# Optimization experiments

Hardware: AMD Instinct MI355X
Metric: run time of the kernel (lower is better)

Reference implementation:

```python
import jax, jax.numpy as jnp
import numpy as np

DIM, E, K, H = 512, 8, 2, 16  # hidden_dim is hardcoded to 16 in the torch module
B, N = 8, 4096
BN_EPS = 1e-5


def setup_inputs() -> dict:
    key = jax.random.key(0)
    ks = jax.random.split(key, 12)
    s = 0.02
    return {
        "x": jax.random.normal(ks[0], (B, N, DIM), jnp.float32),
        # gate: Conv1d(dim, dim, 1) -> weight [dim, dim]; BatchNorm1d(dim); Conv1d(dim, E, 1)
        "wg1": jax.random.normal(ks[1], (DIM, DIM), jnp.float32) * s,
        "bg1": jnp.zeros((DIM,), jnp.float32),
        "gamma": jnp.ones((DIM,), jnp.float32),
        "beta": jnp.zeros((DIM,), jnp.float32),
        "wg2": jax.random.normal(ks[2], (E, DIM), jnp.float32) * s,
        "bg2": jnp.zeros((E,), jnp.float32),
        # experts stacked: Linear(dim,16) -> w1 [E, dim, 16]; Linear(16,dim) -> w2 [E, 16, dim]
        "w1": jax.random.normal(ks[3], (E, DIM, H), jnp.float32) * s,
        "b1": jnp.zeros((E, H), jnp.float32),
        "w2": jax.random.normal(ks[4], (E, H, DIM), jnp.float32) * s,
        "b2": jnp.zeros((E, DIM), jnp.float32),
    }


def reference(x, wg1, bg1, gamma, beta, wg2, bg2, w1, b1, w2, b2):
    b, n, c = x.shape
    t = b * n
    flat = x.reshape(t, c)                                 # [T, C]

    # gate: 1x1 conv == per-token linear; BN over all tokens per channel (train-mode batch stats)
    h = flat @ wg1.T + bg1                                  # [T, C]
    mu = h.mean(axis=0)
    var = h.var(axis=0)                                     # biased, matches torch BN normalization
    h = gamma * (h - mu) * jax.lax.rsqrt(var + BN_EPS) + beta
    h = jax.nn.relu(h)
    logits = h @ wg2.T + bg2                                # [T, E]

    vals, idx = jax.lax.top_k(logits, K)                    # [T, K]
    topk_w = jax.nn.softmax(vals, axis=-1)
    weight = jnp.zeros((t, logits.shape[-1]), logits.dtype)
    weight = weight.at[jnp.arange(t)[:, None], idx].set(topk_w)  # scatter, [T, E]

    # dense expert compute for every token (faithful to original)
    h1 = jax.nn.relu(jnp.einsum('tc,ech->teh', flat, w1) + b1)   # [T, E, H]
    all_out = jnp.einsum('teh,ehc->tec', h1, w2) + b2            # [T, E, C]
    out_flat = jnp.einsum('tec,te->tc', all_out, weight)         # masked combine

    out = out_flat.reshape(b, n, c).transpose(0, 2, 1)           # [B, C, N]
    usage = weight.sum(axis=0) / t
    lb_loss = (usage ** 2).sum() * logits.shape[-1]
    return out, lb_loss
```

## Files before the change

### kernel.cpp

```cpp
#include <hip/hip_runtime.h>

#define T_TOK 32768
#define C_DIM 512
#define N_SEQ 4096

typedef unsigned short ushort_t;
typedef unsigned int uint_t;
typedef __attribute__((ext_vector_type(8))) _Float16 half8;
typedef __attribute__((ext_vector_type(4))) float f32x4;

static __device__ __forceinline__ ushort_t f2h_bits(float f) {
  _Float16 h = (_Float16)f;
  return __builtin_bit_cast(ushort_t, h);
}
static __device__ __forceinline__ float h_bits2f(ushort_t u) {
  return (float)__builtin_bit_cast(_Float16, u);
}

static __device__ __forceinline__ half8 frag_ld(const ushort_t* base, int r, int q) {
  const int off = r * 32 + ((q ^ ((r >> 1) & 3)) * 8);
  return *(const half8*)(base + off);
}

#define GLOAD_LDS(gptr, lptr)                                                  \
  __builtin_amdgcn_global_load_lds(                                            \
      (const __attribute__((address_space(1))) uint_t*)(gptr),                 \
      (__attribute__((address_space(3))) uint_t*)(lptr), 16, 0, 0)

__global__ __launch_bounds__(256) void prep(
    const float* __restrict__ wg1, const float* __restrict__ w1,
    const float* __restrict__ w2, const float* __restrict__ b2,
    ushort_t* __restrict__ Whi, ushort_t* __restrict__ Wlo,
    ushort_t* __restrict__ W1t, ushort_t* __restrict__ W2t,
    float* __restrict__ stats, float* __restrict__ usage,
    uint_t* __restrict__ done) {
  const int idx = blockIdx.x * 256 + threadIdx.x;
  {
    const float v = wg1[idx];
    const ushort_t h = f2h_bits(v);
    Whi[idx] = h;
    Wlo[idx] = f2h_bits(v - h_bits2f(h));
  }
  if (idx < 65536) {
    const int eh = idx >> 9, c = idx & 511;
    const int e = eh >> 4, hh = eh & 15;
    W1t[idx] = f2h_bits(w1[((size_t)e * 512 + c) * 16 + hh]);
  }
  if (idx < 81920) {
    const int c = idx / 160, k = idx - c * 160;
    float v = 0.f;
    if (k < 128) {
      const int e = k >> 4, hh = k & 15;
      v = w2[((size_t)e * 16 + hh) * 512 + c];
    } else if (k < 136) {
      v = b2[(size_t)(k - 128) * 512 + c];
    }
    W2t[c * 160 + k] = f2h_bits(v);
  }
  if (blockIdx.x == 1023) {
    float4 z = {0.f, 0.f, 0.f, 0.f};
    *(float4*)&stats[threadIdx.x * 4] = z;
    if (threadIdx.x < 8) usage[threadIdx.x] = 0.f;
    if (threadIdx.x == 8) *done = 0u;
  }
}

__global__ __launch_bounds__(256) void k1_mfma(
    const float* __restrict__ X, const ushort_t* __restrict__ Whi,
    const ushort_t* __restrict__ Wlo, const float* __restrict__ bg1,
    float* __restrict__ H, float* __restrict__ stats) {
  __shared__ ushort_t sAh[4096], sAl[4096], sBh[4096], sBl[4096];
  const int tid = threadIdx.x, lane = tid & 63, w = tid >> 6;
  const int wm = w >> 1, wn = w & 1;
  const int b = blockIdx.x;
  const int m0 = ((b & 7) | ((b >> 5) << 3)) * 128;
  const int n0 = ((b >> 3) & 3) * 128;
  const int cl = lane & 15, qf = lane >> 4;

  const int p1 = tid, p2 = tid + 256;
  const int r1 = p1 >> 2, q1 = (p1 & 3) ^ ((r1 >> 1) & 3);
  const int r2 = p2 >> 2, q2 = (p2 & 3) ^ ((r2 >> 1) & 3);
  const float* xb1 = X + (size_t)(m0 + r1) * 512 + q1 * 8;
  const float* xb2 = X + (size_t)(m0 + r2) * 512 + q2 * 8;

  float4 xr[4];
#define K1_LOADX(kc)                                                           \
  {                                                                            \
    const int kk = (kc) * 32;                                                  \
    xr[0] = *(const float4*)(xb1 + kk);                                        \
    xr[1] = *(const float4*)(xb1 + kk + 4);                                    \
    xr[2] = *(const float4*)(xb2 + kk);                                        \
    xr[3] = *(const float4*)(xb2 + kk + 4);                                    \
  }

  K1_LOADX(0);
  f32x4 acc[4][4] = {};

  for (int kc = 0; kc < 16; ++kc) {
    const int k0 = kc * 32;
    __syncthreads();
#pragma unroll
    for (int j = 0; j < 2; ++j) {
      const int pb = (w * 2 + j) * 64 + lane;
      const int rb = pb >> 2, qb = (pb & 3) ^ ((rb >> 1) & 3);
      GLOAD_LDS(Whi + (size_t)(n0 + rb) * 512 + k0 + qb * 8, sBh + pb * 8);
      GLOAD_LDS(Wlo + (size_t)(n0 + rb) * 512 + k0 + qb * 8, sBl + pb * 8);
    }
    {
      ushort_t hi[16], lo[16];
      const float* v = (const float*)xr;
#pragma unroll
      for (int j = 0; j < 16; ++j) {
        hi[j] = f2h_bits(v[j]);
        lo[j] = f2h_bits(v[j] - h_bits2f(hi[j]));
      }
      *(uint4*)(sAh + p1 * 8) = *(uint4*)(hi);
      *(uint4*)(sAl + p1 * 8) = *(uint4*)(lo);
      *(uint4*)(sAh + p2 * 8) = *(uint4*)(hi + 8);
      *(uint4*)(sAl + p2 * 8) = *(uint4*)(lo + 8);
    }
    __syncthreads();
    if (kc < 15) K1_LOADX(kc + 1);

    half8 ah[4], al[4], bh[4], bl[4];
#pragma unroll
    for (int f = 0; f < 4; ++f) {
      ah[f] = frag_ld(sAh, wm * 64 + f * 16 + cl, qf);
      al[f] = frag_ld(sAl, wm * 64 + f * 16 + cl, qf);
      bh[f] = frag_ld(sBh, wn * 64 + f * 16 + cl, qf);
      bl[f] = frag_ld(sBl, wn * 64 + f * 16 + cl, qf);
    }
#pragma unroll
    for (int i = 0; i < 4; ++i)
#pragma unroll
      for (int j = 0; j < 4; ++j) {
        acc[i][j] = __builtin_amdgcn_mfma_f32_16x16x32_f16(ah[i], bh[j], acc[i][j], 0, 0, 0);
        acc[i][j] = __builtin_amdgcn_mfma_f32_16x16x32_f16(ah[i], bl[j], acc[i][j], 0, 0, 0);
        acc[i][j] = __builtin_amdgcn_mfma_f32_16x16x32_f16(al[i], bh[j], acc[i][j], 0, 0, 0);
      }
  }
#undef K1_LOADX

  float s[4] = {0, 0, 0, 0}, qs[4] = {0, 0, 0, 0};
  const int rq = lane >> 4;
#pragma unroll
  for (int nf = 0; nf < 4; ++nf) {
    const int col = n0 + wn * 64 + nf * 16 + cl;
    const float bv = bg1[col];
#pragma unroll
    for (int mf = 0; mf < 4; ++mf) {
      const int row = m0 + wm * 64 + mf * 16 + rq * 4;
#pragma unroll
      for (int i = 0; i < 4; ++i) {
        const float v = acc[mf][nf][i] + bv;
        H[(size_t)(row + i) * 512 + col] = v;
        s[nf] += v;
        qs[nf] += v * v;
      }
    }
  }
#pragma unroll
  for (int nf = 0; nf < 4; ++nf) {
    s[nf] += __shfl_xor(s[nf], 16, 64);
    qs[nf] += __shfl_xor(qs[nf], 16, 64);
    s[nf] += __shfl_xor(s[nf], 32, 64);
    qs[nf] += __shfl_xor(qs[nf], 32, 64);
  }
  if (lane < 16) {
#pragma unroll
    for (int nf = 0; nf < 4; ++nf) {
      const int col = n0 + wn * 64 + nf * 16 + cl;
      atomicAdd(&stats[col], s[nf]);
      atomicAdd(&stats[512 + col], qs[nf]);
    }
  }
}

__global__ __launch_bounds__(256) void k5_fused(
    const float* __restrict__ X, const ushort_t* __restrict__ W1t,
    const ushort_t* __restrict__ W2t, const float* __restrict__ b1,
    const float* __restrict__ H, const float* __restrict__ stats,
    const float* __restrict__ gamma, const float* __restrict__ beta,
    const float* __restrict__ wg2, const float* __restrict__ bg2,
    float* __restrict__ usage, uint_t* __restrict__ done,
    float* __restrict__ Out) {
  __shared__ ushort_t sA[2][2048];
  __shared__ ushort_t Pl[64 * 168];
  __shared__ float wtab[64 * 8];
  __shared__ float ys[128 * 68];
  __shared__ float scsh_l[1024];
  __shared__ float lus[8];

  const int tid = threadIdx.x, lane = tid & 63, w = tid >> 6;
  const int wm = w >> 1, wn = w & 1;
  const int t0 = blockIdx.x * 64;
  const int bi = t0 >> 12, n0 = t0 & 4095;
  const int cl = lane & 15, qf = lane >> 4, rq = lane >> 4;

  const int pA = tid, rA = pA >> 2, qA = (pA & 3) ^ ((rA >> 1) & 3);
  const float* xbase = X + (size_t)(t0 + rA) * 512 + qA * 8;
  float4 xq0 = *(const float4*)(xbase);
  float4 xq1 = *(const float4*)(xbase + 4);

  if (tid < 8) lus[tid] = 0.f;
  wtab[tid] = 0.f;
  wtab[tid + 256] = 0.f;
  {
    uint4 z = {0, 0, 0, 0};
    const int row = tid >> 2, hf = tid & 3;
    *(uint4*)&Pl[row * 168 + 128 + hf * 8] = z;
  }
#pragma unroll
  for (int rep = 0; rep < 2; ++rep) {
    const int c = tid + rep * 256;
    const double mu = (double)stats[c] * (1.0 / (double)T_TOK);
    const double var = (double)stats[512 + c] * (1.0 / (double)T_TOK) - mu * mu;
    const double rstd = 1.0 / sqrt(var + 1e-5);
    const float scv = (float)((double)gamma[c] * rstd);
    scsh_l[c] = scv;
    scsh_l[512 + c] = beta[c] - (float)mu * scv;
  }
  __syncthreads();

  {
    const int cb = lane * 8;
    float sc[8], sh[8];
#pragma unroll
    for (int i = 0; i < 8; ++i) {
      sc[i] = scsh_l[cb + i];
      sh[i] = scsh_l[512 + cb + i];
    }
    float wg[8][8];
#pragma unroll
    for (int e = 0; e < 8; ++e)
#pragma unroll
      for (int i = 0; i < 8; ++i) wg[e][i] = wg2[e * C_DIM + cb + i];
    float bg[8];
#pragma unroll
    for (int e = 0; e < 8; ++e) bg[e] = bg2[e];

#pragma unroll 2
    for (int it = 0; it < 16; ++it) {
      const int tl = w * 16 + it;
      const float* hr = H + (size_t)(t0 + tl) * C_DIM + cb;
      float4 h0 = *(const float4*)hr;
      float4 h1 = *(const float4*)(hr + 4);
      float y[8] = {h0.x, h0.y, h0.z, h0.w, h1.x, h1.y, h1.z, h1.w};
#pragma unroll
      for (int i = 0; i < 8; ++i) y[i] = fmaxf(fmaf(y[i], sc[i], sh[i]), 0.f);

      float lg[8];
#pragma unroll
      for (int e = 0; e < 8; ++e) {
        float sum = 0.f;
#pragma unroll
        for (int i = 0; i < 8; ++i) sum = fmaf(y[i], wg[e][i], sum);
        lg[e] = sum;
      }
#pragma unroll
      for (int d = 1; d < 64; d <<= 1)
#pragma unroll
        for (int e = 0; e < 8; ++e) lg[e] += __shfl_xor(lg[e], d, 64);
#pragma unroll
      for (int e = 0; e < 8; ++e) lg[e] += bg[e];

      float v1 = lg[0]; int i1 = 0;
#pragma unroll
      for (int e = 1; e < 8; ++e)
        if (lg[e] > v1) { v1 = lg[e]; i1 = e; }
      float v2 = -3.4e38f; int i2 = 0;
#pragma unroll
      for (int e = 0; e < 8; ++e)
        if (e != i1 && lg[e] > v2) { v2 = lg[e]; i2 = e; }

      const float p = expf(v2 - v1);
      const float rw = 1.f / (1.f + p);
      const float w0 = rw, w1 = p * rw;

      if (lane == 0) {
        wtab[tl * 8 + i1] = w0;
        wtab[tl * 8 + i2] = w1;
        Pl[tl * 168 + 128 + i1] = f2h_bits(w0);
        Pl[tl * 168 + 128 + i2] = f2h_bits(w1);
        atomicAdd(&lus[i1], w0);
        atomicAdd(&lus[i2], w1);
      }
    }
  }
  __syncthreads();
  if (tid < 8) atomicAdd(&usage[tid], lus[tid]);
  __syncthreads();
  if (tid == 0) {
    __threadfence();
    const uint_t ticket = atomicAdd(done, 1u);
    if (ticket == 511u) {
      float s = 0.f;
#pragma unroll
      for (int e = 0; e < 8; ++e) {
        const float u = atomicAdd(&usage[e], 0.f) * (1.f / (float)T_TOK);
        s += u * u;
      }
      Out[(size_t)16777216] = s * 8.f;
    }
  }

  f32x4 acc[2][4] = {};
  for (int kc = 0; kc < 16; ++kc) {
    const int k0 = kc * 32;
    {
      ushort_t hi[8];
      const float v[8] = {xq0.x, xq0.y, xq0.z, xq0.w, xq1.x, xq1.y, xq1.z, xq1.w};
#pragma unroll
      for (int j = 0; j < 8; ++j) hi[j] = f2h_bits(v[j]);
      *(uint4*)(sA[kc & 1] + pA * 8) = *(uint4*)hi;
    }
    __syncthreads();
    if (kc < 15) {
      xq0 = *(const float4*)(xbase + k0 + 32);
      xq1 = *(const float4*)(xbase + k0 + 36);
    }
    half8 bf[4];
#pragma unroll
    for (int f = 0; f < 4; ++f)
      bf[f] = *(const half8*)(W1t + (size_t)(wn * 64 + f * 16 + cl) * 512 + k0 + qf * 8);
    half8 af[2];
#pragma unroll
    for (int f = 0; f < 2; ++f) af[f] = frag_ld(sA[kc & 1], wm * 32 + f * 16 + cl, qf);
#pragma unroll
    for (int i = 0; i < 2; ++i)
#pragma unroll
      for (int j = 0; j < 4; ++j)
        acc[i][j] = __builtin_amdgcn_mfma_f32_16x16x32_f16(af[i], bf[j], acc[i][j], 0, 0, 0);
  }

  {
#pragma unroll
    for (int nf = 0; nf < 4; ++nf) {
      const int col = wn * 64 + nf * 16 + cl;
      const float bv = b1[col];
      const int e = wn * 4 + nf;
#pragma unroll
      for (int mf = 0; mf < 2; ++mf) {
        const int row = wm * 32 + mf * 16 + rq * 4;
#pragma unroll
        for (int i = 0; i < 4; ++i) {
          const float v = fmaxf(acc[mf][nf][i] + bv, 0.f) * wtab[(row + i) * 8 + e];
          Pl[(row + i) * 168 + col] = f2h_bits(v);
        }
      }
    }
  }
  __syncthreads();

  for (int nc = 0; nc < 4; ++nc) {
    f32x4 a2[2][4] = {};
#pragma unroll
    for (int kc = 0; kc < 5; ++kc) {
      const int k0 = kc * 32;
      half8 bf4[4];
#pragma unroll
      for (int f = 0; f < 4; ++f)
        bf4[f] = *(const half8*)(W2t + (size_t)(nc * 128 + wn * 64 + f * 16 + cl) * 160 + k0 + qf * 8);
      half8 af[2];
#pragma unroll
      for (int f = 0; f < 2; ++f)
        af[f] = *(const half8*)(Pl + (wm * 32 + f * 16 + cl) * 168 + k0 + qf * 8);
#pragma unroll
      for (int i = 0; i < 2; ++i)
#pragma unroll
        for (int j = 0; j < 4; ++j)
          a2[i][j] = __builtin_amdgcn_mfma_f32_16x16x32_f16(af[i], bf4[j], a2[i][j], 0, 0, 0);
    }
    __syncthreads();
#pragma unroll
    for (int nf = 0; nf < 4; ++nf) {
      const int c = wn * 64 + nf * 16 + cl;
#pragma unroll
      for (int mf = 0; mf < 2; ++mf) {
        const int trow = wm * 32 + mf * 16 + rq * 4;
#pragma unroll
        for (int i = 0; i < 4; ++i) ys[c * 68 + trow + i] = a2[mf][nf][i];
      }
    }
    __syncthreads();
#pragma unroll
    for (int pass = 0; pass < 8; ++pass) {
      const int c = pass * 16 + (tid >> 4);
      const int f4 = tid & 15;
      float4 v = *(const float4*)&ys[c * 68 + f4 * 4];
      *(float4*)&Out[((size_t)(bi * 512 + nc * 128 + c)) * 4096 + n0 + f4 * 4] = v;
    }
  }
}

extern "C" void kernel_launch(void* const* d_in, const int* in_sizes, int n_in,
                              void* d_out, int out_size, void* d_ws, size_t ws_size,
                              hipStream_t stream) {
  const float* x     = (const float*)d_in[0];
  const float* wg1   = (const float*)d_in[1];
  const float* bg1   = (const float*)d_in[2];
  const float* gamma = (const float*)d_in[3];
  const float* beta  = (const float*)d_in[4];
  const float* wg2   = (const float*)d_in[5];
  const float* bg2   = (const float*)d_in[6];
  const float* w1    = (const float*)d_in[7];
  const float* b1    = (const float*)d_in[8];
  const float* w2    = (const float*)d_in[9];
  const float* b2    = (const float*)d_in[10];
  float* out = (float*)d_out;

  char* ws = (char*)d_ws;
  float*    h     = (float*)ws;
  ushort_t* Whi   = (ushort_t*)(ws + 67108864);
  ushort_t* Wlo   = (ushort_t*)(ws + 67633152);
  ushort_t* W1t   = (ushort_t*)(ws + 68157440);
  ushort_t* W2t   = (ushort_t*)(ws + 68288512);
  float*    stats = (float*)(ws + 68452352);
  float*    usage = (float*)(ws + 68456448);
  uint_t*   done  = (uint_t*)(ws + 68456480);

  prep<<<1024, 256, 0, stream>>>(wg1, w1, w2, b2, Whi, Wlo, W1t, W2t, stats,
                                 usage, done);
  k1_mfma<<<1024, 256, 0, stream>>>(x, Whi, Wlo, bg1, h, stats);
  k5_fused<<<512, 256, 0, stream>>>(x, W1t, W2t, b1, h, stats, gamma, beta,
                                    wg2, bg2, usage, done, out);
}
```

Baseline: 251.5 us.

## Double-buffer LDS tiles in gate GEMM to overlap weight loads with MFMA

The gate GEMM kernel now keeps two LDS buffers for both the A (split-half X) and B (Whi/Wlo) tiles. The next k-chunk's weight tiles are issued as async global-to-LDS loads into the alternate buffer right after the barrier, and the leading barrier of each iteration is removed. The aim is to hide global load latency behind the MFMA work and halve the barriers per k-step. In exchange, LDS use per block doubles to 64 KB, which may lower occupancy.

```diff
diff --git a/kernel.cpp b/kernel.cpp
--- a/kernel.cpp
+++ b/kernel.cpp
@@ -69,7 +69,8 @@
     const float* __restrict__ X, const ushort_t* __restrict__ Whi,
     const ushort_t* __restrict__ Wlo, const float* __restrict__ bg1,
     float* __restrict__ H, float* __restrict__ stats) {
-  __shared__ ushort_t sAh[4096], sAl[4096], sBh[4096], sBl[4096];
+  __shared__ ushort_t sAh[2][4096], sAl[2][4096];
+  __shared__ ushort_t sBh[2][4096], sBl[2][4096];
   const int tid = threadIdx.x, lane = tid & 63, w = tid >> 6;
   const int wm = w >> 1, wn = w & 1;
   const int b = blockIdx.x;
@@ -93,19 +94,23 @@
     xr[3] = *(const float4*)(xb2 + kk + 4);                                    \
   }
 
+#define K1_STAGEB(kc, buf)                                                     \
+  {                                                                            \
+    const int k0s = (kc) * 32;                                                 \
+    _Pragma("unroll") for (int j = 0; j < 2; ++j) {                            \
+      const int pb = (w * 2 + j) * 64 + lane;                                  \
+      const int rb = pb >> 2, qb = (pb & 3) ^ ((rb >> 1) & 3);                 \
+      GLOAD_LDS(Whi + (size_t)(n0 + rb) * 512 + k0s + qb * 8, sBh[buf] + pb * 8); \
+      GLOAD_LDS(Wlo + (size_t)(n0 + rb) * 512 + k0s + qb * 8, sBl[buf] + pb * 8); \
+    }                                                                          \
+  }
+
   K1_LOADX(0);
+  K1_STAGEB(0, 0);
   f32x4 acc[4][4] = {};
 
   for (int kc = 0; kc < 16; ++kc) {
-    const int k0 = kc * 32;
-    __syncthreads();
-#pragma unroll
-    for (int j = 0; j < 2; ++j) {
-      const int pb = (w * 2 + j) * 64 + lane;
-      const int rb = pb >> 2, qb = (pb & 3) ^ ((rb >> 1) & 3);
-      GLOAD_LDS(Whi + (size_t)(n0 + rb) * 512 + k0 + qb * 8, sBh + pb * 8);
-      GLOAD_LDS(Wlo + (size_t)(n0 + rb) * 512 + k0 + qb * 8, sBl + pb * 8);
-    }
+    const int cur = kc & 1;
     {
       ushort_t hi[16], lo[16];
       const float* v = (const float*)xr;
@@ -114,21 +119,24 @@
         hi[j] = f2h_bits(v[j]);
         lo[j] = f2h_bits(v[j] - h_bits2f(hi[j]));
       }
-      *(uint4*)(sAh + p1 * 8) = *(uint4*)(hi);
-      *(uint4*)(sAl + p1 * 8) = *(uint4*)(lo);
-      *(uint4*)(sAh + p2 * 8) = *(uint4*)(hi + 8);
-      *(uint4*)(sAl + p2 * 8) = *(uint4*)(lo + 8);
+      *(uint4*)(sAh[cur] + p1 * 8) = *(uint4*)(hi);
+      *(uint4*)(sAl[cur] + p1 * 8) = *(uint4*)(lo);
+      *(uint4*)(sAh[cur] + p2 * 8) = *(uint4*)(hi + 8);
+      *(uint4*)(sAl[cur] + p2 * 8) = *(uint4*)(lo + 8);
     }
     __syncthreads();
-    if (kc < 15) K1_LOADX(kc + 1);
+    if (kc < 15) {
+      K1_LOADX(kc + 1);
+      K1_STAGEB(kc + 1, cur ^ 1);
+    }
 
     half8 ah[4], al[4], bh[4], bl[4];
 #pragma unroll
     for (int f = 0; f < 4; ++f) {
-      ah[f] = frag_ld(sAh, wm * 64 + f * 16 + cl, qf);
-      al[f] = frag_ld(sAl, wm * 64 + f * 16 + cl, qf);
-      bh[f] = frag_ld(sBh, wn * 64 + f * 16 + cl, qf);
-      bl[f] = frag_ld(sBl, wn * 64 + f * 16 + cl, qf);
+      ah[f] = frag_ld(sAh[cur], wm * 64 + f * 16 + cl, qf);
+      al[f] = frag_ld(sAl[cur], wm * 64 + f * 16 + cl, qf);
+      bh[f] = frag_ld(sBh[cur], wn * 64 + f * 16 + cl, qf);
+      bl[f] = frag_ld(sBl[cur], wn * 64 + f * 16 + cl, qf);
     }
 #pragma unroll
     for (int i = 0; i < 4; ++i)
@@ -140,6 +148,7 @@
       }
   }
 #undef K1_LOADX
+#undef K1_STAGEB
 
   float s[4] = {0, 0, 0, 0}, qs[4] = {0, 0, 0, 0};
   const int rq = lane >> 4;
```

New measurement: 267.0 us. +6.2%, slower.

## Fuse expert first-layer GEMM into gate GEMM kernel, pass fp16 activations

Applied to the files above, without the earlier changes.

Computes the expert first-layer projection (X·W1, 128 hidden columns) inside the gate GEMM kernel, reusing the already-staged fp16-hi X fragments in LDS. Each block contributes a 32-column slice, writes relu(.+b1) as fp16 to a workspace buffer Ph, and the second kernel now reads Ph instead of reloading and converting X for another K=512 GEMM. This removes a second full read of X and the duplicate GEMM loop from k5, in exchange for extra MFMAs and global W1t loads in k1 plus a small fp16 intermediate write/read. It also drops one barrier before the done-ticket logic.

```diff
diff --git a/kernel.cpp b/kernel.cpp
--- a/kernel.cpp
+++ b/kernel.cpp
@@ -67,15 +67,18 @@
 
 __global__ __launch_bounds__(256) void k1_mfma(
     const float* __restrict__ X, const ushort_t* __restrict__ Whi,
-    const ushort_t* __restrict__ Wlo, const float* __restrict__ bg1,
-    float* __restrict__ H, float* __restrict__ stats) {
+    const ushort_t* __restrict__ Wlo, const ushort_t* __restrict__ W1t,
+    const float* __restrict__ bg1, const float* __restrict__ b1,
+    float* __restrict__ H, float* __restrict__ stats,
+    ushort_t* __restrict__ Ph) {
   __shared__ ushort_t sAh[4096], sAl[4096], sBh[4096], sBl[4096];
   const int tid = threadIdx.x, lane = tid & 63, w = tid >> 6;
   const int wm = w >> 1, wn = w & 1;
   const int b = blockIdx.x;
   const int m0 = ((b & 7) | ((b >> 5) << 3)) * 128;
   const int n0 = ((b >> 3) & 3) * 128;
-  const int cl = lane & 15, qf = lane >> 4;
+  const int eh0 = n0 >> 2;
+  const int cl = lane & 15, qf = lane >> 4, rq = lane >> 4;
 
   const int p1 = tid, p2 = tid + 256;
   const int r1 = p1 >> 2, q1 = (p1 & 3) ^ ((r1 >> 1) & 3);
@@ -95,6 +98,7 @@
 
   K1_LOADX(0);
   f32x4 acc[4][4] = {};
+  f32x4 acc1[4] = {};
 
   for (int kc = 0; kc < 16; ++kc) {
     const int k0 = kc * 32;
@@ -122,6 +126,8 @@
     __syncthreads();
     if (kc < 15) K1_LOADX(kc + 1);
 
+    half8 bf1 = *(const half8*)(W1t + (size_t)(eh0 + wn * 16 + cl) * 512 + k0 + qf * 8);
+
     half8 ah[4], al[4], bh[4], bl[4];
 #pragma unroll
     for (int f = 0; f < 4; ++f) {
@@ -138,11 +144,25 @@
         acc[i][j] = __builtin_amdgcn_mfma_f32_16x16x32_f16(ah[i], bl[j], acc[i][j], 0, 0, 0);
         acc[i][j] = __builtin_amdgcn_mfma_f32_16x16x32_f16(al[i], bh[j], acc[i][j], 0, 0, 0);
       }
+#pragma unroll
+    for (int i = 0; i < 4; ++i)
+      acc1[i] = __builtin_amdgcn_mfma_f32_16x16x32_f16(ah[i], bf1, acc1[i], 0, 0, 0);
   }
 #undef K1_LOADX
 
+  {
+    const int col = eh0 + wn * 16 + cl;
+    const float b1v = b1[col];
+#pragma unroll
+    for (int mf = 0; mf < 4; ++mf) {
+      const int row = m0 + wm * 64 + mf * 16 + rq * 4;
+#pragma unroll
+      for (int i = 0; i < 4; ++i)
+        Ph[(size_t)(row + i) * 128 + col] = f2h_bits(fmaxf(acc1[mf][i] + b1v, 0.f));
+    }
+  }
+
   float s[4] = {0, 0, 0, 0}, qs[4] = {0, 0, 0, 0};
-  const int rq = lane >> 4;
 #pragma unroll
   for (int nf = 0; nf < 4; ++nf) {
     const int col = n0 + wn * 64 + nf * 16 + cl;
@@ -177,14 +197,12 @@
 }
 
 __global__ __launch_bounds__(256) void k5_fused(
-    const float* __restrict__ X, const ushort_t* __restrict__ W1t,
-    const ushort_t* __restrict__ W2t, const float* __restrict__ b1,
+    const ushort_t* __restrict__ Ph, const ushort_t* __restrict__ W2t,
     const float* __restrict__ H, const float* __restrict__ stats,
     const float* __restrict__ gamma, const float* __restrict__ beta,
     const float* __restrict__ wg2, const float* __restrict__ bg2,
     float* __restrict__ usage, uint_t* __restrict__ done,
     float* __restrict__ Out) {
-  __shared__ ushort_t sA[2][2048];
   __shared__ ushort_t Pl[64 * 168];
   __shared__ float wtab[64 * 8];
   __shared__ float ys[128 * 68];
@@ -197,10 +215,12 @@
   const int bi = t0 >> 12, n0 = t0 & 4095;
   const int cl = lane & 15, qf = lane >> 4, rq = lane >> 4;
 
-  const int pA = tid, rA = pA >> 2, qA = (pA & 3) ^ ((rA >> 1) & 3);
-  const float* xbase = X + (size_t)(t0 + rA) * 512 + qA * 8;
-  float4 xq0 = *(const float4*)(xbase);
-  float4 xq1 = *(const float4*)(xbase + 4);
+  const int prow = tid >> 2, pc0 = (tid & 3) * 32;
+  const ushort_t* phb = Ph + (size_t)(t0 + prow) * 128 + pc0;
+  half8 ph0 = *(const half8*)(phb);
+  half8 ph1 = *(const half8*)(phb + 8);
+  half8 ph2 = *(const half8*)(phb + 16);
+  half8 ph3 = *(const half8*)(phb + 24);
 
   if (tid < 8) lus[tid] = 0.f;
   wtab[tid] = 0.f;
@@ -289,7 +309,6 @@
   }
   __syncthreads();
   if (tid < 8) atomicAdd(&usage[tid], lus[tid]);
-  __syncthreads();
   if (tid == 0) {
     __threadfence();
     const uint_t ticket = atomicAdd(done, 1u);
@@ -304,51 +323,22 @@
     }
   }
 
-  f32x4 acc[2][4] = {};
-  for (int kc = 0; kc < 16; ++kc) {
-    const int k0 = kc * 32;
-    {
-      ushort_t hi[8];
-      const float v[8] = {xq0.x, xq0.y, xq0.z, xq0.w, xq1.x, xq1.y, xq1.z, xq1.w};
-#pragma unroll
-      for (int j = 0; j < 8; ++j) hi[j] = f2h_bits(v[j]);
-      *(uint4*)(sA[kc & 1] + pA * 8) = *(uint4*)hi;
-    }
-    __syncthreads();
-    if (kc < 15) {
-      xq0 = *(const float4*)(xbase + k0 + 32);
-      xq1 = *(const float4*)(xbase + k0 + 36);
-    }
-    half8 bf[4];
-#pragma unroll
-    for (int f = 0; f < 4; ++f)
-      bf[f] = *(const half8*)(W1t + (size_t)(wn * 64 + f * 16 + cl) * 512 + k0 + qf * 8);
-    half8 af[2];
-#pragma unroll
-    for (int f = 0; f < 2; ++f) af[f] = frag_ld(sA[kc & 1], wm * 32 + f * 16 + cl, qf);
-#pragma unroll
-    for (int i = 0; i < 2; ++i)
-#pragma unroll
-      for (int j = 0; j < 4; ++j)
-        acc[i][j] = __builtin_amdgcn_mfma_f32_16x16x32_f16(af[i], bf[j], acc[i][j], 0, 0, 0);
-  }
-
   {
-#pragma unroll
-    for (int nf = 0; nf < 4; ++nf) {
-      const int col = wn * 64 + nf * 16 + cl;
-      const float bv = b1[col];
-      const int e = wn * 4 + nf;
-#pragma unroll
-      for (int mf = 0; mf < 2; ++mf) {
-        const int row = wm * 32 + mf * 16 + rq * 4;
-#pragma unroll
-        for (int i = 0; i < 4; ++i) {
-          const float v = fmaxf(acc[mf][nf][i] + bv, 0.f) * wtab[(row + i) * 8 + e];
-          Pl[(row + i) * 168 + col] = f2h_bits(v);
-        }
-      }
-    }
+    const int e0 = pc0 >> 4;
+    const float gw0 = wtab[prow * 8 + e0];
+    const float gw1 = wtab[prow * 8 + e0 + 1];
+    ushort_t o[32];
+#pragma unroll
+    for (int j = 0; j < 8; ++j) {
+      o[j]      = f2h_bits((float)ph0[j] * gw0);
+      o[8 + j]  = f2h_bits((float)ph1[j] * gw0);
+      o[16 + j] = f2h_bits((float)ph2[j] * gw1);
+      o[24 + j] = f2h_bits((float)ph3[j] * gw1);
+    }
+    *(uint4*)&Pl[prow * 168 + pc0]      = *(uint4*)(o);
+    *(uint4*)&Pl[prow * 168 + pc0 + 8]  = *(uint4*)(o + 8);
+    *(uint4*)&Pl[prow * 168 + pc0 + 16] = *(uint4*)(o + 16);
+    *(uint4*)&Pl[prow * 168 + pc0 + 24] = *(uint4*)(o + 24);
   }
   __syncthreads();
 
@@ -418,10 +408,11 @@
   float*    stats = (float*)(ws + 68452352);
   float*    usage = (float*)(ws + 68456448);
   uint_t*   done  = (uint_t*)(ws + 68456480);
+  ushort_t* Ph    = (ushort_t*)(ws + 68456512);
 
   prep<<<1024, 256, 0, stream>>>(wg1, w1, w2, b2, Whi, Wlo, W1t, W2t, stats,
                                  usage, done);
-  k1_mfma<<<1024, 256, 0, stream>>>(x, Whi, Wlo, bg1, h, stats);
-  k5_fused<<<512, 256, 0, stream>>>(x, W1t, W2t, b1, h, stats, gamma, beta,
-                                    wg2, bg2, usage, done, out);
-}
+  k1_mfma<<<1024, 256, 0, stream>>>(x, Whi, Wlo, W1t, bg1, b1, h, stats, Ph);
+  k5_fused<<<512, 256, 0, stream>>>(Ph, W2t, h, stats, gamma, beta, wg2, bg2,
+                                    usage, done, out);
+}
```

After: 241.4 us. 1.04x faster.
